# Optimization experiments

Measured on AMD Instinct MI355X. Metric: run time of the kernel, lower is better.

## Reference

```python
import jax, jax.numpy as jnp
import numpy as np

NSTEP, NGRID = 365, 50000
PRECS = 1e-05
# [lo, hi] physical ranges for the first 12 HBV parameters (routing params unused, routOpt=False)
PARA_RANGES = np.array([
    [1, 6], [50, 1000], [0.05, 0.9], [0.01, 0.5], [0.001, 0.2], [0.2, 1],
    [0, 10], [0, 100], [-2.5, 2.5], [0.5, 10], [0, 0.1], [0, 0.2],
], dtype=np.float32)


def setup_inputs() -> dict:
    key = jax.random.key(0)
    k1, k2 = jax.random.split(key)
    x = jax.random.uniform(k1, (NSTEP, NGRID, 3), dtype=jnp.float32)
    parameters = jax.random.uniform(k2, (NGRID, 14), dtype=jnp.float32)
    return {"x": x, "parameters": parameters}


def _hbv_forward(x, parameters):
    P = x[:, :, 0]       # precip   [Nstep, Ngrid]
    T = x[:, :, 1]       # temp
    ETpot = x[:, :, 2]   # potential ET
    lo = jnp.asarray(PARA_RANGES[:, 0])
    hi = jnp.asarray(PARA_RANGES[:, 1])
    p = lo + parameters[:, :12] * (hi - lo)  # [Ngrid, 12]
    (parBETA, parFC, parK0, parK1, parK2, parLP, parPERC, parUZL,
     parTT, parCFMAX, parCFR, parCWH) = [p[:, i] for i in range(12)]

    ngrid = P.shape[1]
    init = tuple(jnp.full((ngrid,), 0.001, dtype=jnp.float32) for _ in range(5))

    def step(carry, inp):
        SNOWPACK, MELTWATER, SM, SUZ, SLZ = carry
        PRECIP, Tt, ETp = inp
        is_rain = (Tt >= parTT).astype(jnp.float32)
        RAIN = PRECIP * is_rain
        SNOW = PRECIP * (1.0 - is_rain)
        SNOWPACK = SNOWPACK + SNOW
        melt = jnp.minimum(jnp.maximum(parCFMAX * (Tt - parTT), 0.0), SNOWPACK)
        MELTWATER = MELTWATER + melt
        SNOWPACK = SNOWPACK - melt
        refreezing = jnp.minimum(jnp.maximum(parCFR * parCFMAX * (parTT - Tt), 0.0), MELTWATER)
        SNOWPACK = SNOWPACK + refreezing
        MELTWATER = MELTWATER - refreezing
        tosoil = jnp.maximum(MELTWATER - parCWH * SNOWPACK, 0.0)
        MELTWATER = MELTWATER - tosoil
        soil_wetness = jnp.clip((SM / parFC) ** parBETA, 0.0, 1.0)
        recharge = (RAIN + tosoil) * soil_wetness
        SM = SM + RAIN + tosoil - recharge
        excess = jnp.maximum(SM - parFC, 0.0)
        SM = SM - excess
        evapfactor = jnp.clip(SM / (parLP * parFC), 0.0, 1.0)
        ETact = jnp.minimum(SM, ETp * evapfactor)
        SM = jnp.maximum(SM - ETact, PRECS)
        SUZ = SUZ + recharge + excess
        PERC = jnp.minimum(SUZ, parPERC)
        SUZ = SUZ - PERC
        Q0 = parK0 * jnp.maximum(SUZ - parUZL, 0.0)
        SUZ = SUZ - Q0
        Q1 = parK1 * SUZ
        SUZ = SUZ - Q1
        SLZ = SLZ + PERC
        Q2 = parK2 * SLZ
        SLZ = SLZ - Q2
        return (SNOWPACK, MELTWATER, SM, SUZ, SLZ), Q0 + Q1 + Q2

    _, Qsim = jax.lax.scan(step, init, (P, T, ETpot))
    return Qsim[..., None]  # [Nstep, Ngrid, 1]


def reference(x, parameters):
    return _hbv_forward(x, parameters)
```

## Files before the change

### kernel.cpp

```cpp
#include <hip/hip_runtime.h>

#define NSTEP 365
#define NGRID 50000
#define PRECS_F 1e-5f
#define CHUNK 16

#if defined(__has_builtin)
#  if __has_builtin(__builtin_amdgcn_exp2f) && __has_builtin(__builtin_amdgcn_logf)
#    define FAST_EXP2(x) __builtin_amdgcn_exp2f(x)
#    define FAST_LOG2(x) __builtin_amdgcn_logf(x)
#  endif
#endif
#ifndef FAST_EXP2
#  define FAST_EXP2(x) exp2f(x)
#  define FAST_LOG2(x) log2f(x)
#endif

__global__ __launch_bounds__(64) void hbv_kernel(const float* __restrict__ x,
                                                 const float* __restrict__ params,
                                                 float* __restrict__ out) {
    const int g = blockIdx.x * blockDim.x + threadIdx.x;
    if (g >= NGRID) return;

    const float* pr = params + (size_t)g * 14;
    float r0 = pr[0], r1 = pr[1], r2 = pr[2], r3 = pr[3], r4 = pr[4], r5 = pr[5];
    float r6 = pr[6], r7 = pr[7], r8 = pr[8], r9 = pr[9], r10 = pr[10], r11 = pr[11];

    const float parBETA  = 1.0f   + r0  * 5.0f;
    const float parFC    = 50.0f  + r1  * 950.0f;
    const float parK0    = 0.05f  + r2  * 0.85f;
    const float parK1    = 0.01f  + r3  * 0.49f;
    const float parK2    = 0.001f + r4  * 0.199f;
    const float parLP    = 0.2f   + r5  * 0.8f;
    const float parPERC  =          r6  * 10.0f;
    const float parUZL   =          r7  * 100.0f;
    const float parTT    = -2.5f  + r8  * 5.0f;
    const float parCFMAX = 0.5f   + r9  * 9.5f;
    const float parCFR   =          r10 * 0.1f;
    const float parCWH   =          r11 * 0.2f;

    const float invFC     = 1.0f / parFC;
    const float invLPFC   = 1.0f / (parLP * parFC);
    const float cfr_cfmax = parCFR * parCFMAX;

    float SNOWPACK = 0.001f, MELTWATER = 0.001f, SM = 0.001f, SUZ = 0.001f, SLZ = 0.001f;

    const int nchunks = (NSTEP + CHUNK - 1) / CHUNK;

    float AP[CHUNK], AT[CHUNK], AE[CHUNK];
    float BP[CHUNK], BT[CHUNK], BE[CHUNK];

    auto load_chunk = [&](int cidx, float (&P)[CHUNK], float (&T)[CHUNK], float (&E)[CHUNK]) {
        const int tbase = cidx * CHUNK;
        #pragma unroll
        for (int j = 0; j < CHUNK; ++j) {
            int t = tbase + j;
            t = (t < NSTEP) ? t : (NSTEP - 1);
            const float* p = x + ((size_t)t * NGRID + g) * 3;
            P[j] = p[0];
            T[j] = p[1];
            E[j] = p[2];
        }
    };

    auto compute_chunk = [&](int cidx, const float (&P)[CHUNK], const float (&T)[CHUNK],
                             const float (&E)[CHUNK]) {
        const int t0 = cidx * CHUNK;
        #pragma unroll
        for (int j = 0; j < CHUNK; ++j) {
            const float PRECIP = P[j];
            const float Tt     = T[j];
            const float ETp    = E[j];

            float RAIN = (Tt >= parTT) ? PRECIP : 0.0f;
            float SNOW = PRECIP - RAIN;
            SNOWPACK += SNOW;
            float melt = fminf(fmaxf(parCFMAX * (Tt - parTT), 0.0f), SNOWPACK);
            MELTWATER += melt;
            SNOWPACK  -= melt;
            float refreeze = fminf(fmaxf(cfr_cfmax * (parTT - Tt), 0.0f), MELTWATER);
            SNOWPACK  += refreeze;
            MELTWATER -= refreeze;
            float tosoil = fmaxf(MELTWATER - parCWH * SNOWPACK, 0.0f);
            MELTWATER -= tosoil;

            float ratio = SM * invFC;
            float sw = FAST_EXP2(parBETA * FAST_LOG2(ratio));
            sw = fminf(fmaxf(sw, 0.0f), 1.0f);
            float recharge = (RAIN + tosoil) * sw;
            SM += RAIN + tosoil - recharge;
            float excess = fmaxf(SM - parFC, 0.0f);
            SM -= excess;
            float evapfactor = fminf(fmaxf(SM * invLPFC, 0.0f), 1.0f);
            float ETact = fminf(SM, ETp * evapfactor);
            SM = fmaxf(SM - ETact, PRECS_F);

            SUZ += recharge + excess;
            float PERC = fminf(SUZ, parPERC);
            SUZ -= PERC;
            float Q0 = parK0 * fmaxf(SUZ - parUZL, 0.0f);
            SUZ -= Q0;
            float Q1 = parK1 * SUZ;
            SUZ -= Q1;
            SLZ += PERC;
            float Q2 = parK2 * SLZ;
            SLZ -= Q2;

            const int t = t0 + j;
            if (t < NSTEP) out[(size_t)t * NGRID + g] = Q0 + Q1 + Q2;
        }
    };

    load_chunk(0, AP, AT, AE);
    int c = 0;
    for (;;) {
        if (c + 1 < nchunks) load_chunk(c + 1, BP, BT, BE);
        compute_chunk(c, AP, AT, AE);
        if (++c >= nchunks) break;
        if (c + 1 < nchunks) load_chunk(c + 1, AP, AT, AE);
        compute_chunk(c, BP, BT, BE);
        if (++c >= nchunks) break;
    }
}

extern "C" void kernel_launch(void* const* d_in, const int* in_sizes, int n_in,
                              void* d_out, int out_size, void* d_ws, size_t ws_size,
                              hipStream_t stream) {
    const float* x      = (const float*)d_in[0];
    const float* params = (const float*)d_in[1];
    float* out          = (float*)d_out;

    const int block = 64;
    const int grid  = (NGRID + block - 1) / block;
    hbv_kernel<<<grid, block, 0, stream>>>(x, params, out);
}
```

Baseline: 324.0 us.

## Stage input chunks via global_load_lds double buffer with explicit waitcnt

Replaces the register-array double buffering of forcing inputs with direct global-to-LDS asynchronous loads into a two-slot LDS buffer, using explicit vmcnt waits so the next chunk's 48 loads stay in flight while the current chunk computes. Out-of-range lanes are clamped rather than exiting early so all lanes take part in the LDS loads. This aims to cut register pressure and let loads overlap compute more reliably. It relies on hand-encoded waitcnt values and the vmcnt counter limits on this architecture, which is fragile if the counter encoding or the load count doesn't match.

```diff
diff --git a/kernel.cpp b/kernel.cpp
--- a/kernel.cpp
+++ b/kernel.cpp
@@ -4,40 +4,47 @@
 #define NGRID 50000
 #define PRECS_F 1e-5f
 #define CHUNK 16
+#define NCHUNK ((NSTEP + CHUNK - 1) / CHUNK)
 
 #if defined(__has_builtin)
 #  if __has_builtin(__builtin_amdgcn_exp2f) && __has_builtin(__builtin_amdgcn_logf)
-#    define FAST_EXP2(x) __builtin_amdgcn_exp2f(x)
-#    define FAST_LOG2(x) __builtin_amdgcn_logf(x)
+#    define FAST_EXP2(v) __builtin_amdgcn_exp2f(v)
+#    define FAST_LOG2(v) __builtin_amdgcn_logf(v)
 #  endif
 #endif
 #ifndef FAST_EXP2
-#  define FAST_EXP2(x) exp2f(x)
-#  define FAST_LOG2(x) log2f(x)
+#  define FAST_EXP2(v) exp2f(v)
+#  define FAST_LOG2(v) log2f(v)
 #endif
+
+#define WAITCNT_VM48 0xCF70
+#define WAITCNT_VM0  0x0F70
+
+typedef const void __attribute__((address_space(1)))* gas_cptr;
+typedef void __attribute__((address_space(3)))*       las_ptr;
 
 __global__ __launch_bounds__(64) void hbv_kernel(const float* __restrict__ x,
                                                  const float* __restrict__ params,
                                                  float* __restrict__ out) {
-    const int g = blockIdx.x * blockDim.x + threadIdx.x;
-    if (g >= NGRID) return;
+    __shared__ float lds[2][CHUNK][3][64];
 
-    const float* pr = params + (size_t)g * 14;
-    float r0 = pr[0], r1 = pr[1], r2 = pr[2], r3 = pr[3], r4 = pr[4], r5 = pr[5];
-    float r6 = pr[6], r7 = pr[7], r8 = pr[8], r9 = pr[9], r10 = pr[10], r11 = pr[11];
+    const int lane = threadIdx.x;
+    const int g    = blockIdx.x * 64 + lane;
+    const int gg   = (g < NGRID) ? g : (NGRID - 1);
 
-    const float parBETA  = 1.0f   + r0  * 5.0f;
-    const float parFC    = 50.0f  + r1  * 950.0f;
-    const float parK0    = 0.05f  + r2  * 0.85f;
-    const float parK1    = 0.01f  + r3  * 0.49f;
-    const float parK2    = 0.001f + r4  * 0.199f;
-    const float parLP    = 0.2f   + r5  * 0.8f;
-    const float parPERC  =          r6  * 10.0f;
-    const float parUZL   =          r7  * 100.0f;
-    const float parTT    = -2.5f  + r8  * 5.0f;
-    const float parCFMAX = 0.5f   + r9  * 9.5f;
-    const float parCFR   =          r10 * 0.1f;
-    const float parCWH   =          r11 * 0.2f;
+    const float* pr = params + (size_t)gg * 14;
+    const float parBETA  = 1.0f   + pr[0]  * 5.0f;
+    const float parFC    = 50.0f  + pr[1]  * 950.0f;
+    const float parK0    = 0.05f  + pr[2]  * 0.85f;
+    const float parK1    = 0.01f  + pr[3]  * 0.49f;
+    const float parK2    = 0.001f + pr[4]  * 0.199f;
+    const float parLP    = 0.2f   + pr[5]  * 0.8f;
+    const float parPERC  =          pr[6]  * 10.0f;
+    const float parUZL   =          pr[7]  * 100.0f;
+    const float parTT    = -2.5f  + pr[8]  * 5.0f;
+    const float parCFMAX = 0.5f   + pr[9]  * 9.5f;
+    const float parCFR   =          pr[10] * 0.1f;
+    const float parCWH   =          pr[11] * 0.2f;
 
     const float invFC     = 1.0f / parFC;
     const float invLPFC   = 1.0f / (parLP * parFC);
@@ -45,32 +52,28 @@
 
     float SNOWPACK = 0.001f, MELTWATER = 0.001f, SM = 0.001f, SUZ = 0.001f, SLZ = 0.001f;
 
-    const int nchunks = (NSTEP + CHUNK - 1) / CHUNK;
-
-    float AP[CHUNK], AT[CHUNK], AE[CHUNK];
-    float BP[CHUNK], BT[CHUNK], BE[CHUNK];
-
-    auto load_chunk = [&](int cidx, float (&P)[CHUNK], float (&T)[CHUNK], float (&E)[CHUNK]) {
+    auto stage = [&](int cidx) {
+        const int b     = cidx & 1;
         const int tbase = cidx * CHUNK;
         #pragma unroll
         for (int j = 0; j < CHUNK; ++j) {
             int t = tbase + j;
             t = (t < NSTEP) ? t : (NSTEP - 1);
-            const float* p = x + ((size_t)t * NGRID + g) * 3;
-            P[j] = p[0];
-            T[j] = p[1];
-            E[j] = p[2];
+            const float* gp = x + ((size_t)t * NGRID + gg) * 3;
+            __builtin_amdgcn_global_load_lds((gas_cptr)(gp + 0), (las_ptr)&lds[b][j][0][0], 4, 0, 0);
+            __builtin_amdgcn_global_load_lds((gas_cptr)(gp + 1), (las_ptr)&lds[b][j][1][0], 4, 0, 0);
+            __builtin_amdgcn_global_load_lds((gas_cptr)(gp + 2), (las_ptr)&lds[b][j][2][0], 4, 0, 0);
         }
     };
 
-    auto compute_chunk = [&](int cidx, const float (&P)[CHUNK], const float (&T)[CHUNK],
-                             const float (&E)[CHUNK]) {
+    auto compute = [&](int cidx) {
+        const int b  = cidx & 1;
         const int t0 = cidx * CHUNK;
         #pragma unroll
         for (int j = 0; j < CHUNK; ++j) {
-            const float PRECIP = P[j];
-            const float Tt     = T[j];
-            const float ETp    = E[j];
+            const float PRECIP = lds[b][j][0][lane];
+            const float Tt     = lds[b][j][1][lane];
+            const float ETp    = lds[b][j][2][lane];
 
             float RAIN = (Tt >= parTT) ? PRECIP : 0.0f;
             float SNOW = PRECIP - RAIN;
@@ -107,19 +110,21 @@
             SLZ -= Q2;
 
             const int t = t0 + j;
-            if (t < NSTEP) out[(size_t)t * NGRID + g] = Q0 + Q1 + Q2;
+            if (t < NSTEP && g < NGRID)
+                out[(size_t)t * NGRID + g] = Q0 + Q1 + Q2;
         }
     };
 
-    load_chunk(0, AP, AT, AE);
-    int c = 0;
-    for (;;) {
-        if (c + 1 < nchunks) load_chunk(c + 1, BP, BT, BE);
-        compute_chunk(c, AP, AT, AE);
-        if (++c >= nchunks) break;
-        if (c + 1 < nchunks) load_chunk(c + 1, AP, AT, AE);
-        compute_chunk(c, BP, BT, BE);
-        if (++c >= nchunks) break;
+    stage(0);
+    for (int c = 0; c < NCHUNK; ++c) {
+        if (c + 1 < NCHUNK) {
+            stage(c + 1);
+            __builtin_amdgcn_s_waitcnt(WAITCNT_VM48);
+        } else {
+            __builtin_amdgcn_s_waitcnt(WAITCNT_VM0);
+        }
+        asm volatile("" ::: "memory");
+        compute(c);
     }
 }
 
```

Result: slower. 338.2 us (+4.4%).
